# Kernel tuning notes

Measured on AMD Instinct MI355X. Metric: run time of the kernel, lower is better.

## Reference

```python
import jax, jax.numpy as jnp
import numpy as np

N_NODES = 100000
N_EDGES = 1600000
IN_C = 128
OUT_C = 128


def setup_inputs() -> dict:
    key = jax.random.key(0)
    k1, k2, k3, k4 = jax.random.split(key, 4)
    x = jax.random.normal(k1, (N_NODES, IN_C), dtype=jnp.float32)
    W = jax.random.normal(k2, (IN_C, OUT_C), dtype=jnp.float32) * (1.0 / np.sqrt(IN_C))
    b = jax.random.normal(k3, (OUT_C,), dtype=jnp.float32) * 0.02
    edge_index = jax.random.randint(k4, (2, N_EDGES), 0, N_NODES, dtype=jnp.int32)
    return {"x": x, "W": W, "b": b, "edge_index": edge_index}


def reference(x, W, b, edge_index):
    N = x.shape[0]
    # Symmetrize edges: concat(edge_index, flip(edge_index)) as in adj()
    row = jnp.concatenate([edge_index[0], edge_index[1]])  # [2E]
    col = jnp.concatenate([edge_index[1], edge_index[0]])  # [2E]
    w = jnp.ones(row.shape, dtype=x.dtype)
    # gcn_norm with self loops (fill value 1): deg includes self-loop weight
    deg = jax.ops.segment_sum(w, row, num_segments=N) + 1.0
    dinv = jnp.where(deg > 0, jax.lax.rsqrt(deg), 0.0)  # [N]
    # Dense linear projection (bias=False)
    xw = x @ W  # [N, out]
    # SpMM: y[row] += dinv[row]*dinv[col] * xw[col]  (scatter-add == coalesced adj matmul)
    norm = dinv[row] * dinv[col]  # [2E]
    msgs = norm[:, None] * xw[col]  # [2E, out] -- dominant memory traffic
    y = jax.ops.segment_sum(msgs, row, num_segments=N)
    # Self-loop contribution: weight dinv[i]^2
    y = y + (dinv * dinv)[:, None] * xw
    return y + b
```

## Files before the change

### kernel.cpp

```cpp
#include <hip/hip_runtime.h>
#include <math.h>

constexpr int N = 100000;
constexpr int E = 1600000;
constexpr int C = 128;
constexpr int NBUCK = 64;
constexpr int NPB   = (N + NBUCK - 1) / NBUCK;
constexpr int CAP   = 53248;

__device__ inline unsigned f2bf(float f) {
    unsigned u = __float_as_uint(f);
    return (u + 0x7fffu + ((u >> 16) & 1u)) >> 16;
}
__device__ inline unsigned pack2(float lo, float hi) {
    return f2bf(lo) | (f2bf(hi) << 16);
}
__device__ inline float bf_lo(unsigned m) { return __uint_as_float(m << 16); }
__device__ inline float bf_hi(unsigned m) { return __uint_as_float(m & 0xffff0000u); }

__global__ __launch_bounds__(256) void k_bin(const int* __restrict__ ei,
                                             int* __restrict__ gcount,
                                             unsigned* __restrict__ staging) {
    __shared__ int cnt[NBUCK];
    __shared__ int wbase[NBUCK];
    const int t = threadIdx.x;
    const long tile = (long)blockIdx.x * 2048;
    if (t < NBUCK) cnt[t] = 0;
    __syncthreads();
    int b0[8], b1[8], lo0[8], lo1[8];
    unsigned p0[8], p1[8];
    bool val[8];
#pragma unroll
    for (int j = 0; j < 8; ++j) {
        long e = tile + j * 256 + t;
        val[j] = e < E;
        if (val[j]) {
            int u = __builtin_nontemporal_load(ei + e);
            int v = __builtin_nontemporal_load(ei + E + e);
            b0[j] = u / NPB;
            b1[j] = v / NPB;
            p0[j] = ((unsigned)(u - b0[j] * NPB) << 17) | (unsigned)v;
            p1[j] = ((unsigned)(v - b1[j] * NPB) << 17) | (unsigned)u;
            lo0[j] = atomicAdd(&cnt[b0[j]], 1);
            lo1[j] = atomicAdd(&cnt[b1[j]], 1);
        }
    }
    __syncthreads();
    if (t < NBUCK) wbase[t] = atomicAdd(&gcount[t], cnt[t]);
    __syncthreads();
#pragma unroll
    for (int j = 0; j < 8; ++j) {
        if (val[j]) {
            staging[(size_t)b0[j] * CAP + wbase[b0[j]] + lo0[j]] = p0[j];
            staging[(size_t)b1[j] * CAP + wbase[b1[j]] + lo1[j]] = p1[j];
        }
    }
}

__global__ __launch_bounds__(512) void k_csr(const unsigned* __restrict__ staging,
                                             const int* __restrict__ gcount,
                                             int* __restrict__ deg,
                                             float* __restrict__ dinv,
                                             int* __restrict__ rowptr,
                                             int* __restrict__ adj) {
    __shared__ int hist[2049];
    __shared__ int wpart[8];
    __shared__ int sh_base;
    const int g = blockIdx.x;
    const int t = threadIdx.x;
    const int cnt = gcount[g];
    if (t == 0) {
        int s = 0;
        for (int i = 0; i < g; ++i) s += gcount[i];
        sh_base = s;
    }
    for (int i = t; i < 2049; i += 512) hist[i] = 0;
    __syncthreads();
    const unsigned* base = staging + (size_t)g * CAP;
    for (int i = t; i < cnt; i += 512) atomicAdd(&hist[base[i] >> 17], 1);
    __syncthreads();
    const int i4 = t * 4;
    const int a0 = hist[i4], a1 = hist[i4 + 1], a2 = hist[i4 + 2], a3 = hist[i4 + 3];
    const int s = a0 + a1 + a2 + a3;
    const int lane = t & 63, wid = t >> 6;
    int v = s;
#pragma unroll
    for (int off = 1; off < 64; off <<= 1) {
        int n = __shfl_up(v, off);
        if (lane >= off) v += n;
    }
    if (lane == 63) wpart[wid] = v;
    __syncthreads();
    if (t == 0) {
        int r = 0;
#pragma unroll
        for (int w = 0; w < 8; ++w) { int x = wpart[w]; wpart[w] = r; r += x; }
    }
    __syncthreads();
    const int excl = v - s + wpart[wid];
    hist[i4]     = excl;
    hist[i4 + 1] = excl + a0;
    hist[i4 + 2] = excl + a0 + a1;
    hist[i4 + 3] = excl + a0 + a1 + a2;
    __syncthreads();
    const int nbase = g * NPB;
    const int nlocal = min(NPB, N - nbase);
    const int bbase = sh_base;
    for (int i = t; i < nlocal; i += 512) {
        int st = hist[i], en = hist[i + 1];
        int d = en - st;
        deg[nbase + i] = d;
        dinv[nbase + i] = rsqrtf((float)d + 1.0f);
        rowptr[nbase + i] = bbase + st;
    }
    __syncthreads();
    int* aslice = adj + bbase;
    for (int i = t; i < cnt; i += 512) {
        unsigned e = base[i];
        int pos = atomicAdd(&hist[e >> 17], 1);
        aslice[pos] = (int)(e & 0x1ffffu);
    }
}

__global__ __launch_bounds__(256) void k_gemm(const float* __restrict__ x,
                                              const float* __restrict__ W,
                                              unsigned* __restrict__ xw16) {
    __shared__ float Ws[32][128];
    __shared__ float xs[64][33];

    const int t   = threadIdx.x;
    const int r0  = (t & 15) * 4;
    const int c0  = (t >> 4) * 8;
    const int bid = blockIdx.x;

    float acc[4][8];
#pragma unroll
    for (int i = 0; i < 4; ++i)
#pragma unroll
        for (int j = 0; j < 8; ++j) acc[i][j] = 0.0f;

    const int lrow = t >> 2;
    const int lk   = (t & 3) * 8;
    const long grow = (long)bid * 64 + lrow;
    const bool rvalid = grow < N;

    for (int k0 = 0; k0 < C; k0 += 32) {
        const float4* Wg = (const float4*)(W + (size_t)k0 * C);
        float4* Wsv = (float4*)(&Ws[0][0]);
#pragma unroll
        for (int j = 0; j < 4; ++j) Wsv[t + 256 * j] = Wg[t + 256 * j];
        float4 a0 = {0, 0, 0, 0}, a1 = {0, 0, 0, 0};
        if (rvalid) {
            a0 = *(const float4*)(x + grow * C + k0 + lk);
            a1 = *(const float4*)(x + grow * C + k0 + lk + 4);
        }
        xs[lrow][lk + 0] = a0.x; xs[lrow][lk + 1] = a0.y;
        xs[lrow][lk + 2] = a0.z; xs[lrow][lk + 3] = a0.w;
        xs[lrow][lk + 4] = a1.x; xs[lrow][lk + 5] = a1.y;
        xs[lrow][lk + 6] = a1.z; xs[lrow][lk + 7] = a1.w;
        __syncthreads();

#pragma unroll 8
        for (int k = 0; k < 32; ++k) {
            float4 w0 = *(const float4*)&Ws[k][c0];
            float4 w1 = *(const float4*)&Ws[k][c0 + 4];
            float xv[4];
#pragma unroll
            for (int i = 0; i < 4; ++i) xv[i] = xs[r0 + i][k];
#pragma unroll
            for (int i = 0; i < 4; ++i) {
                acc[i][0] = fmaf(xv[i], w0.x, acc[i][0]);
                acc[i][1] = fmaf(xv[i], w0.y, acc[i][1]);
                acc[i][2] = fmaf(xv[i], w0.z, acc[i][2]);
                acc[i][3] = fmaf(xv[i], w0.w, acc[i][3]);
                acc[i][4] = fmaf(xv[i], w1.x, acc[i][4]);
                acc[i][5] = fmaf(xv[i], w1.y, acc[i][5]);
                acc[i][6] = fmaf(xv[i], w1.z, acc[i][6]);
                acc[i][7] = fmaf(xv[i], w1.w, acc[i][7]);
            }
        }
        __syncthreads();
    }

#pragma unroll
    for (int i = 0; i < 4; ++i) {
        long r = (long)bid * 64 + r0 + i;
        if (r >= N) break;
        uint4 pk = {pack2(acc[i][0], acc[i][1]), pack2(acc[i][2], acc[i][3]),
                    pack2(acc[i][4], acc[i][5]), pack2(acc[i][6], acc[i][7])};
        *(uint4*)(xw16 + r * (C / 2) + (c0 >> 1)) = pk;
    }
}

__global__ __launch_bounds__(256) void k_gather(const int* __restrict__ rowptr,
                                                const int* __restrict__ deg,
                                                const float* __restrict__ dinv,
                                                const int* __restrict__ adj,
                                                const unsigned* __restrict__ xw16,
                                                const float* __restrict__ b,
                                                float* __restrict__ out) {
    int u = blockIdx.x * 4 + (threadIdx.x >> 6);
    if (u >= N) return;
    const int lane = threadIdx.x & 63;
    const int d = deg[u];
    const int start = rowptr[u];
    const float du = dinv[u];
    const unsigned ms = xw16[(size_t)u * (C / 2) + lane];
    const float2 bb = *(const float2*)(b + 2 * lane);
    const float s2 = du * du;
    float ax = fmaf(s2, bf_lo(ms), bb.x);
    float ay = fmaf(s2, bf_hi(ms), bb.y);

    for (int j0 = 0; j0 < d; j0 += 64) {
        int v = 0;
        float dv = 0.f;
        if (j0 + lane < d) {
            v = adj[start + j0 + lane];
            dv = dinv[v];
        }
        const int cnt = min(64, d - j0);
        int jj = 0;
        for (; jj + 4 <= cnt; jj += 4) {
            int v0 = __shfl(v, jj),     v1 = __shfl(v, jj + 1);
            int v2 = __shfl(v, jj + 2), v3 = __shfl(v, jj + 3);
            float w0 = du * __shfl(dv, jj),     w1 = du * __shfl(dv, jj + 1);
            float w2 = du * __shfl(dv, jj + 2), w3 = du * __shfl(dv, jj + 3);
            unsigned m0 = xw16[(size_t)v0 * (C / 2) + lane];
            unsigned m1 = xw16[(size_t)v1 * (C / 2) + lane];
            unsigned m2 = xw16[(size_t)v2 * (C / 2) + lane];
            unsigned m3 = xw16[(size_t)v3 * (C / 2) + lane];
            ax = fmaf(w0, bf_lo(m0), ax); ay = fmaf(w0, bf_hi(m0), ay);
            ax = fmaf(w1, bf_lo(m1), ax); ay = fmaf(w1, bf_hi(m1), ay);
            ax = fmaf(w2, bf_lo(m2), ax); ay = fmaf(w2, bf_hi(m2), ay);
            ax = fmaf(w3, bf_lo(m3), ax); ay = fmaf(w3, bf_hi(m3), ay);
        }
        for (; jj < cnt; ++jj) {
            int vv = __shfl(v, jj);
            float w = du * __shfl(dv, jj);
            unsigned m = xw16[(size_t)vv * (C / 2) + lane];
            ax = fmaf(w, bf_lo(m), ax);
            ay = fmaf(w, bf_hi(m), ay);
        }
    }
    float2 o = {ax, ay};
    *(float2*)(out + (size_t)u * C + 2 * lane) = o;
}

extern "C" void kernel_launch(void* const* d_in, const int* in_sizes, int n_in,
                              void* d_out, int out_size, void* d_ws, size_t ws_size,
                              hipStream_t stream) {
    const float* x  = (const float*)d_in[0];
    const float* W  = (const float*)d_in[1];
    const float* b  = (const float*)d_in[2];
    const int*   ei = (const int*)d_in[3];
    float* out = (float*)d_out;

    char* p = (char*)d_ws;
    unsigned* xw16 = (unsigned*)p;  p += (size_t)N * (C / 2) * sizeof(unsigned);
    int* deg = (int*)p;             p += (size_t)N * sizeof(int);
    float* dinv = (float*)p;        p += (size_t)N * sizeof(float);
    int* rowptr = (int*)p;          p += (size_t)(N + 4) * sizeof(int);
    int* gcount = (int*)p;          p += 256 * sizeof(int);
    unsigned* staging = (unsigned*)p; p += (size_t)NBUCK * CAP * sizeof(unsigned);
    int* adj = (int*)p;

    hipMemsetAsync(gcount, 0, 256 * sizeof(int), stream);
    k_bin<<<(E + 2047) / 2048, 256, 0, stream>>>(ei, gcount, staging);
    k_csr<<<NBUCK, 512, 0, stream>>>(staging, gcount, deg, dinv, rowptr, adj);
    k_gemm<<<(N + 63) / 64, 256, 0, stream>>>(x, W, xw16);
    k_gather<<<(N + 3) / 4, 256, 0, stream>>>(rowptr, deg, dinv, adj, xw16, b, out);
}
```

Baseline: 356.8 us.

## Prescale projection by dinv, use finer CSR buckets, simplify gather loop

```diff
diff --git a/kernel.cpp b/kernel.cpp
--- a/kernel.cpp
+++ b/kernel.cpp
@@ -4,9 +4,9 @@
 constexpr int N = 100000;
 constexpr int E = 1600000;
 constexpr int C = 128;
-constexpr int NBUCK = 64;
-constexpr int NPB   = (N + NBUCK - 1) / NBUCK;
-constexpr int CAP   = 53248;
+constexpr int NPB   = 256;
+constexpr int NBUCK = (N + NPB - 1) / NPB;
+constexpr int CAP   = 9472;
 
 __device__ inline unsigned f2bf(float f) {
     unsigned u = __float_as_uint(f);
@@ -25,7 +25,7 @@
     __shared__ int wbase[NBUCK];
     const int t = threadIdx.x;
     const long tile = (long)blockIdx.x * 2048;
-    if (t < NBUCK) cnt[t] = 0;
+    for (int i = t; i < NBUCK; i += 256) cnt[i] = 0;
     __syncthreads();
     int b0[8], b1[8], lo0[8], lo1[8];
     unsigned p0[8], p1[8];
@@ -37,16 +37,16 @@
         if (val[j]) {
             int u = __builtin_nontemporal_load(ei + e);
             int v = __builtin_nontemporal_load(ei + E + e);
-            b0[j] = u / NPB;
-            b1[j] = v / NPB;
-            p0[j] = ((unsigned)(u - b0[j] * NPB) << 17) | (unsigned)v;
-            p1[j] = ((unsigned)(v - b1[j] * NPB) << 17) | (unsigned)u;
+            b0[j] = u >> 8;
+            b1[j] = v >> 8;
+            p0[j] = ((unsigned)(u & 255) << 17) | (unsigned)v;
+            p1[j] = ((unsigned)(v & 255) << 17) | (unsigned)u;
             lo0[j] = atomicAdd(&cnt[b0[j]], 1);
             lo1[j] = atomicAdd(&cnt[b1[j]], 1);
         }
     }
     __syncthreads();
-    if (t < NBUCK) wbase[t] = atomicAdd(&gcount[t], cnt[t]);
+    for (int i = t; i < NBUCK; i += 256) wbase[i] = atomicAdd(&gcount[i], cnt[i]);
     __syncthreads();
 #pragma unroll
     for (int j = 0; j < 8; ++j) {
@@ -63,68 +63,70 @@
                                              float* __restrict__ dinv,
                                              int* __restrict__ rowptr,
                                              int* __restrict__ adj) {
-    __shared__ int hist[2049];
+    __shared__ int hist[NPB + 1];
     __shared__ int wpart[8];
+    __shared__ int wsum[8];
     __shared__ int sh_base;
     const int g = blockIdx.x;
     const int t = threadIdx.x;
+    const int lane = t & 63, wid = t >> 6;
     const int cnt = gcount[g];
+    int s = (t < g) ? gcount[t] : 0;
+#pragma unroll
+    for (int off = 32; off; off >>= 1) s += __shfl_down(s, off);
+    if (lane == 0) wsum[wid] = s;
+    for (int i = t; i <= NPB; i += 512) hist[i] = 0;
+    __syncthreads();
     if (t == 0) {
-        int s = 0;
-        for (int i = 0; i < g; ++i) s += gcount[i];
-        sh_base = s;
-    }
-    for (int i = t; i < 2049; i += 512) hist[i] = 0;
-    __syncthreads();
+        int r = 0;
+#pragma unroll
+        for (int w = 0; w < 8; ++w) r += wsum[w];
+        sh_base = r;
+    }
     const unsigned* base = staging + (size_t)g * CAP;
     for (int i = t; i < cnt; i += 512) atomicAdd(&hist[base[i] >> 17], 1);
     __syncthreads();
-    const int i4 = t * 4;
-    const int a0 = hist[i4], a1 = hist[i4 + 1], a2 = hist[i4 + 2], a3 = hist[i4 + 3];
-    const int s = a0 + a1 + a2 + a3;
-    const int lane = t & 63, wid = t >> 6;
-    int v = s;
+    const int a = (t < NPB) ? hist[t] : 0;
+    int v = a;
 #pragma unroll
     for (int off = 1; off < 64; off <<= 1) {
         int n = __shfl_up(v, off);
         if (lane >= off) v += n;
     }
-    if (lane == 63) wpart[wid] = v;
+    if (lane == 63 && wid < NPB / 64) wpart[wid] = v;
     __syncthreads();
     if (t == 0) {
         int r = 0;
 #pragma unroll
-        for (int w = 0; w < 8; ++w) { int x = wpart[w]; wpart[w] = r; r += x; }
-    }
-    __syncthreads();
-    const int excl = v - s + wpart[wid];
-    hist[i4]     = excl;
-    hist[i4 + 1] = excl + a0;
-    hist[i4 + 2] = excl + a0 + a1;
-    hist[i4 + 3] = excl + a0 + a1 + a2;
+        for (int w = 0; w < NPB / 64; ++w) { int x = wpart[w]; wpart[w] = r; r += x; }
+    }
+    __syncthreads();
+    if (t < NPB) hist[t] = v - a + wpart[wid];
+    if (t == 0) hist[NPB] = cnt;
     __syncthreads();
     const int nbase = g * NPB;
     const int nlocal = min(NPB, N - nbase);
     const int bbase = sh_base;
-    for (int i = t; i < nlocal; i += 512) {
-        int st = hist[i], en = hist[i + 1];
-        int d = en - st;
-        deg[nbase + i] = d;
-        dinv[nbase + i] = rsqrtf((float)d + 1.0f);
-        rowptr[nbase + i] = bbase + st;
+    if (t < nlocal) {
+        const int st = hist[t], en = hist[t + 1];
+        const int d = en - st;
+        deg[nbase + t] = d;
+        dinv[nbase + t] = rsqrtf((float)d + 1.0f);
+        rowptr[nbase + t] = bbase + st;
     }
     __syncthreads();
     int* aslice = adj + bbase;
     for (int i = t; i < cnt; i += 512) {
-        unsigned e = base[i];
-        int pos = atomicAdd(&hist[e >> 17], 1);
+        const unsigned e = base[i];
+        const int pos = atomicAdd(&hist[e >> 17], 1);
         aslice[pos] = (int)(e & 0x1ffffu);
     }
 }
 
 __global__ __launch_bounds__(256) void k_gemm(const float* __restrict__ x,
                                               const float* __restrict__ W,
-                                              unsigned* __restrict__ xw16) {
+                                              const float* __restrict__ dinv,
+                                              unsigned* __restrict__ z16) {
     __shared__ float Ws[32][128];
     __shared__ float xs[64][33];
 
@@ -186,9 +188,10 @@
     for (int i = 0; i < 4; ++i) {
         long r = (long)bid * 64 + r0 + i;
         if (r >= N) break;
-        uint4 pk = {pack2(acc[i][0], acc[i][1]), pack2(acc[i][2], acc[i][3]),
-                    pack2(acc[i][4], acc[i][5]), pack2(acc[i][6], acc[i][7])};
-        *(uint4*)(xw16 + r * (C / 2) + (c0 >> 1)) = pk;
+        const float dv = dinv[r];
+        uint4 pk = {pack2(dv * acc[i][0], dv * acc[i][1]), pack2(dv * acc[i][2], dv * acc[i][3]),
+                    pack2(dv * acc[i][4], dv * acc[i][5]), pack2(dv * acc[i][6], dv * acc[i][7])};
+        *(uint4*)(z16 + r * (C / 2) + (c0 >> 1)) = pk;
     }
 }
 
@@ -196,53 +199,59 @@
                                                 const int* __restrict__ deg,
                                                 const float* __restrict__ dinv,
                                                 const int* __restrict__ adj,
-                                                const unsigned* __restrict__ xw16,
+                                                const unsigned* __restrict__ z16,
                                                 const float* __restrict__ b,
                                                 float* __restrict__ out) {
-    int u = blockIdx.x * 4 + (threadIdx.x >> 6);
+    const int u = blockIdx.x * 4 + (threadIdx.x >> 6);
     if (u >= N) return;
     const int lane = threadIdx.x & 63;
-    const int d = deg[u];
-    const int start = rowptr[u];
+    const int d  = __builtin_amdgcn_readfirstlane(deg[u]);
+    const int st = __builtin_amdgcn_readfirstlane(rowptr[u]);
     const float du = dinv[u];
-    const unsigned ms = xw16[(size_t)u * (C / 2) + lane];
-    const float2 bb = *(const float2*)(b + 2 * lane);
-    const float s2 = du * du;
-    float ax = fmaf(s2, bf_lo(ms), bb.x);
-    float ay = fmaf(s2, bf_hi(ms), bb.y);
+    const unsigned ms = z16[((unsigned)u << 6) + lane];
+    float ax0 = bf_lo(ms), ay0 = bf_hi(ms);
+    float ax1 = 0.f, ay1 = 0.f;
 
     for (int j0 = 0; j0 < d; j0 += 64) {
         int v = 0;
-        float dv = 0.f;
-        if (j0 + lane < d) {
-            v = adj[start + j0 + lane];
-            dv = dinv[v];
-        }
-        const int cnt = min(64, d - j0);
+        if (j0 + lane < d) v = adj[st + j0 + lane];
+        const int cntc = min(64, d - j0);
         int jj = 0;
-        for (; jj + 4 <= cnt; jj += 4) {
-            int v0 = __shfl(v, jj),     v1 = __shfl(v, jj + 1);
-            int v2 = __shfl(v, jj + 2), v3 = __shfl(v, jj + 3);
-            float w0 = du * __shfl(dv, jj),     w1 = du * __shfl(dv, jj + 1);
-            float w2 = du * __shfl(dv, jj + 2), w3 = du * __shfl(dv, jj + 3);
-            unsigned m0 = xw16[(size_t)v0 * (C / 2) + lane];
-            unsigned m1 = xw16[(size_t)v1 * (C / 2) + lane];
-            unsigned m2 = xw16[(size_t)v2 * (C / 2) + lane];
-            unsigned m3 = xw16[(size_t)v3 * (C / 2) + lane];
-            ax = fmaf(w0, bf_lo(m0), ax); ay = fmaf(w0, bf_hi(m0), ay);
-            ax = fmaf(w1, bf_lo(m1), ax); ay = fmaf(w1, bf_hi(m1), ay);
-            ax = fmaf(w2, bf_lo(m2), ax); ay = fmaf(w2, bf_hi(m2), ay);
-            ax = fmaf(w3, bf_lo(m3), ax); ay = fmaf(w3, bf_hi(m3), ay);
-        }
-        for (; jj < cnt; ++jj) {
-            int vv = __shfl(v, jj);
-            float w = du * __shfl(dv, jj);
-            unsigned m = xw16[(size_t)vv * (C / 2) + lane];
-            ax = fmaf(w, bf_lo(m), ax);
-            ay = fmaf(w, bf_hi(m), ay);
-        }
-    }
-    float2 o = {ax, ay};
+        for (; jj + 8 <= cntc; jj += 8) {
+            const int v0 = __builtin_amdgcn_readlane(v, jj + 0);
+            const int v1 = __builtin_amdgcn_readlane(v, jj + 1);
+            const int v2 = __builtin_amdgcn_readlane(v, jj + 2);
+            const int v3 = __builtin_amdgcn_readlane(v, jj + 3);
+            const int v4 = __builtin_amdgcn_readlane(v, jj + 4);
+            const int v5 = __builtin_amdgcn_readlane(v, jj + 5);
+            const int v6 = __builtin_amdgcn_readlane(v, jj + 6);
+            const int v7 = __builtin_amdgcn_readlane(v, jj + 7);
+            const unsigned m0 = (z16 + (((size_t)(unsigned)v0) << 6))[lane];
+            const unsigned m1 = (z16 + (((size_t)(unsigned)v1) << 6))[lane];
+            const unsigned m2 = (z16 + (((size_t)(unsigned)v2) << 6))[lane];
+            const unsigned m3 = (z16 + (((size_t)(unsigned)v3) << 6))[lane];
+            const unsigned m4 = (z16 + (((size_t)(unsigned)v4) << 6))[lane];
+            const unsigned m5 = (z16 + (((size_t)(unsigned)v5) << 6))[lane];
+            const unsigned m6 = (z16 + (((size_t)(unsigned)v6) << 6))[lane];
+            const unsigned m7 = (z16 + (((size_t)(unsigned)v7) << 6))[lane];
+            ax0 += bf_lo(m0); ay0 += bf_hi(m0);
+            ax1 += bf_lo(m1); ay1 += bf_hi(m1);
+            ax0 += bf_lo(m2); ay0 += bf_hi(m2);
+            ax1 += bf_lo(m3); ay1 += bf_hi(m3);
+            ax0 += bf_lo(m4); ay0 += bf_hi(m4);
+            ax1 += bf_lo(m5); ay1 += bf_hi(m5);
+            ax0 += bf_lo(m6); ay0 += bf_hi(m6);
+            ax1 += bf_lo(m7); ay1 += bf_hi(m7);
+        }
+        for (; jj < cntc; ++jj) {
+            const int vv = __builtin_amdgcn_readlane(v, jj);
+            const unsigned m = (z16 + (((size_t)(unsigned)vv) << 6))[lane];
+            ax0 += bf_lo(m); ay0 += bf_hi(m);
+        }
+    }
+    const float2 bb = *(const float2*)(b + 2 * lane);
+    const float ax = ax0 + ax1, ay = ay0 + ay1;
+    float2 o = {fmaf(du, ax, bb.x), fmaf(du, ay, bb.y)};
     *(float2*)(out + (size_t)u * C + 2 * lane) = o;
 }
 
@@ -256,17 +265,17 @@
     float* out = (float*)d_out;
 
     char* p = (char*)d_ws;
-    unsigned* xw16 = (unsigned*)p;  p += (size_t)N * (C / 2) * sizeof(unsigned);
+    unsigned* z16 = (unsigned*)p;   p += (size_t)N * (C / 2) * sizeof(unsigned);
     int* deg = (int*)p;             p += (size_t)N * sizeof(int);
     float* dinv = (float*)p;        p += (size_t)N * sizeof(float);
     int* rowptr = (int*)p;          p += (size_t)(N + 4) * sizeof(int);
-    int* gcount = (int*)p;          p += 256 * sizeof(int);
+    int* gcount = (int*)p;          p += 512 * sizeof(int);
     unsigned* staging = (unsigned*)p; p += (size_t)NBUCK * CAP * sizeof(unsigned);
     int* adj = (int*)p;
 
-    hipMemsetAsync(gcount, 0, 256 * sizeof(int), stream);
+    hipMemsetAsync(gcount, 0, 512 * sizeof(int), stream);
     k_bin<<<(E + 2047) / 2048, 256, 0, stream>>>(ei, gcount, staging);
     k_csr<<<NBUCK, 512, 0, stream>>>(staging, gcount, deg, dinv, rowptr, adj);
-    k_gemm<<<(N + 63) / 64, 256, 0, stream>>>(x, W, xw16);
-    k_gather<<<(N + 3) / 4, 256, 0, stream>>>(rowptr, deg, dinv, adj, xw16, b, out);
-}
+    k_gemm<<<(N + 63) / 64, 256, 0, stream>>>(x, W, dinv, z16);
+    k_gather<<<(N + 3) / 4, 256, 0, stream>>>(rowptr, deg, dinv, adj, z16, b, out);
+}
```

After: 324.6 us. 1.1x faster.
